# Kernel tuning notes

Measured on AMD Instinct MI355X. Metric: run time of the kernel, lower is better.

## Reference

```python
import jax, jax.numpy as jnp
import numpy as np

EPS = 1e-5  # config.layer_norm_epsilon

def setup_inputs() -> dict:
    key = jax.random.key(0)
    ks = jax.random.split(key, 3)
    B, S, NX, A, H, O = 16, 2048, 1024, 20, 50, 3
    x = jax.random.normal(ks[0], (B, S, NX), dtype=jnp.float32)
    ln_g = jnp.ones((A, NX), jnp.float32)
    ln_b = jnp.zeros((A, NX), jnp.float32)
    W1 = jax.random.normal(ks[1], (A, NX, H), dtype=jnp.float32) * (1.0 / np.sqrt(NX))
    b1 = jnp.zeros((A, H), jnp.float32)
    W2 = jax.random.normal(ks[2], (A, H, O), dtype=jnp.float32) * (1.0 / np.sqrt(H))
    b2 = jnp.zeros((A, O), jnp.float32)
    return {"x": x, "ln_g": ln_g, "ln_b": ln_b, "W1": W1, "b1": b1, "W2": W2, "b2": b2}

def reference(x, ln_g, ln_b, W1, b1, W2, b2):
    B, S, NX = x.shape
    A = ln_g.shape[0]
    # shared normalization (per-token mean/var), per-adapter affine folded into W1
    mu = jnp.mean(x, axis=-1, keepdims=True)
    var = jnp.mean(jnp.square(x - mu), axis=-1, keepdims=True)  # biased, like torch LN
    xn = (x - mu) * jax.lax.rsqrt(var + EPS)                    # [B,S,NX]
    W1g = ln_g[:, :, None] * W1                                 # [A,NX,H], absorbs LN gamma
    off = jnp.einsum('an,anh->ah', ln_b, W1) + b1               # [A,H],   absorbs LN beta
    h = jax.nn.relu(jnp.einsum('bsn,anh->bash', xn, W1g) + off[None, :, None, :])  # [B,A,S,H]
    o = jnp.einsum('bash,aho->baso', h, W2) + b2[None, :, None, :]                 # [B,A,S,3]
    out = o.reshape(B, A, S * o.shape[-1])                      # [B,A,S*3] (row-major == torch view)
    # squash over the adapter/capsule axis (dim=-1 of [B,S*3,A] == axis 1 here)
    sq = jnp.sum(jnp.square(out), axis=1, keepdims=True)
    scale = sq / (1.0 + sq)
    return scale * out * jax.lax.rsqrt(sq)
```

## Files before the change

### kernel.cpp

```cpp
#include <hip/hip_runtime.h>
#include <hip/hip_bf16.h>
#include <stdint.h>


typedef _Float16 h8 __attribute__((ext_vector_type(8)));
typedef float f4 __attribute__((ext_vector_type(4)));
typedef __attribute__((address_space(1))) void gvoid;
typedef __attribute__((address_space(3))) void lvoid;

__device__ __forceinline__ void cp16(const void* g, void* l) {
  __builtin_amdgcn_global_load_lds((gvoid*)g, (lvoid*)l, 16, 0, 0);
}

__global__ __launch_bounds__(256) void pre_kernel(
    const float* __restrict__ x, const float* __restrict__ ln_g,
    const float* __restrict__ ln_b, const float* __restrict__ W1,
    _Float16* __restrict__ wB, float* __restrict__ offpart,
    float* __restrict__ out, _Float16* __restrict__ xn) {
  const int t = threadIdx.x;
  if (blockIdx.x >= 432) {
    const int w = t >> 6, l = t & 63;
    const int tok = (blockIdx.x - 432) * 4 + w;
    const float4* xr = (const float4*)(x + (size_t)tok * 1024);
    float4 v0 = xr[l], v1 = xr[64 + l], v2 = xr[128 + l], v3 = xr[192 + l];
    float s1 = (v0.x + v0.y + v0.z + v0.w) + (v1.x + v1.y + v1.z + v1.w) +
               (v2.x + v2.y + v2.z + v2.w) + (v3.x + v3.y + v3.z + v3.w);
    float s2 = v0.x * v0.x + v0.y * v0.y + v0.z * v0.z + v0.w * v0.w;
    s2 += v1.x * v1.x + v1.y * v1.y + v1.z * v1.z + v1.w * v1.w;
    s2 += v2.x * v2.x + v2.y * v2.y + v2.z * v2.z + v2.w * v2.w;
    s2 += v3.x * v3.x + v3.y * v3.y + v3.z * v3.z + v3.w * v3.w;
#pragma unroll
    for (int m = 32; m > 0; m >>= 1) {
      s1 += __shfl_xor(s1, m);
      s2 += __shfl_xor(s2, m);
    }
    const float mu = s1 * 0.0009765625f;
    const float var = s2 * 0.0009765625f - mu * mu;
    const float inv = rsqrtf(var + 1e-5f);
    uint2* xw = (uint2*)(xn + (size_t)tok * 1024);
    union { _Float16 h[4]; uint2 u; } q;
#define CVT_STORE(V, OFF)                                 \
    q.h[0] = (_Float16)((V.x - mu) * inv);                \
    q.h[1] = (_Float16)((V.y - mu) * inv);                \
    q.h[2] = (_Float16)((V.z - mu) * inv);                \
    q.h[3] = (_Float16)((V.w - mu) * inv);                \
    xw[(OFF) + l] = q.u;
    CVT_STORE(v0, 0)
    CVT_STORE(v1, 64)
    CVT_STORE(v2, 128)
    CVT_STORE(v3, 192)
#undef CVT_STORE
    return;
  }
  if (blockIdx.x >= 320) {
    static const int sa[7] = {2, 5, 7, 10, 12, 15, 17};
    const int idx = blockIdx.x - 320;
    const int ai = idx >> 4, bi = idx & 15;
    float4* dst = (float4*)(out + ((size_t)(bi * 20 + sa[ai])) * 6144);
    const float4 z4 = {0.f, 0.f, 0.f, 0.f};
    for (int i = t; i < 1536; i += 256) dst[i] = z4;
    return;
  }
  const int a = blockIdx.x >> 4, k0 = (blockIdx.x & 15) * 64;
  __shared__ float tw[3200];
  __shared__ float gg[64], bb[64], red[256];
  const float* src = W1 + (size_t)(a * 1024 + k0) * 50;
  for (int i = t; i < 3200; i += 256) tw[i] = src[i];
  if (t < 64) gg[t] = ln_g[a * 1024 + k0 + t];
  else if (t < 128) bb[t - 64] = ln_b[a * 1024 + k0 + (t - 64)];
  __syncthreads();
  const int h = t & 63, q = t >> 6;
  float po = 0.f;
  if (h < 50) {
#pragma unroll
    for (int half = 0; half < 2; ++half) {
      union { _Float16 hh[8]; uint4 u; } pk;
#pragma unroll
      for (int j = 0; j < 8; ++j) {
        const int k = q * 16 + half * 8 + j;
        const float wv = tw[k * 50 + h];
        pk.hh[j] = (_Float16)(gg[k] * wv);
        po += bb[k] * wv;
      }
      *(uint4*)(wB + (size_t)(a * 50 + h) * 1024 + k0 + q * 16 + half * 8) =
          pk.u;
    }
  }
  red[t] = po;
  __syncthreads();
  if (t < 50)
    offpart[(blockIdx.x & 15) * 1024 + a * 50 + t] =
        red[t] + red[64 + t] + red[128 + t] + red[192 + t];
  if (a == 0 && t < 192) {
    const uint4 z = {0, 0, 0, 0};
    *(uint4*)(wB + (size_t)(1000 + (t >> 3)) * 1024 + k0 + (t & 7) * 8) = z;
  }
}

__global__ __launch_bounds__(256, 4) void gemm_kernel(
    const _Float16* __restrict__ xn, const _Float16* __restrict__ wB,
    const float* __restrict__ offpart, const float* __restrict__ b1,
    const float* __restrict__ W2, float* __restrict__ out) {
  __shared__ __align__(16) char smem[36448];
  const int g = blockIdx.x;
  const int xcd = g & 7, i0 = g >> 3;
  const int nb = i0 & 7;
  const int mb = xcd * 32 + (i0 >> 3);
  const int t = threadIdx.x, w = t >> 6, l = t & 63;

  const int a0 = (nb * 128) / 50;
  float* w2s = (float*)(smem + 34048);
  for (int i = t; i < 600; i += 256) {
    const int j = i / 150, a = a0 + j;
    w2s[i] = (a < 20) ? W2[a * 150 + (i - j * 150)] : 0.f;
  }

  const int lr = l >> 3;
  const int ksl = (l & 7) ^ lr;
  const _Float16* gA = xn + (size_t)(mb * 128 + lr) * 1024 + ksl * 8;
  const _Float16* gB = wB + (size_t)(nb * 128 + lr) * 1024 + ksl * 8;

  const int rowA = ((w >> 1) * 64) + (l & 15);
  const int rowB = ((w & 1) * 64) + (l & 15);
  const int kq = l >> 4;
  const int xa = rowA & 7, xb = rowB & 7;
  const char* pA = smem + rowA * 128;
  const char* pB = smem + 16384 + rowB * 128;

  f4 acc[4][4];
  {
    f4 z = {0.f, 0.f, 0.f, 0.f};
#pragma unroll
    for (int mt = 0; mt < 4; ++mt)
#pragma unroll
      for (int nt = 0; nt < 4; ++nt) acc[mt][nt] = z;
  }

  for (int kt = 0; kt < 16; ++kt) {
#pragma unroll
    for (int i = 0; i < 4; ++i) {
      const int chunk = w * 4 + i;
      cp16(gA + (size_t)chunk * 8192 + kt * 64, smem + chunk * 1024);
      cp16(gB + (size_t)chunk * 8192 + kt * 64, smem + 16384 + chunk * 1024);
    }
    __syncthreads();
#pragma unroll
    for (int ks = 0; ks < 2; ++ks) {
      h8 af[4], bf[4];
      const int sl = ks * 4 + kq;
#pragma unroll
      for (int mt = 0; mt < 4; ++mt)
        af[mt] = *(const h8*)(pA + mt * 2048 + ((sl ^ xa) << 4));
#pragma unroll
      for (int nt = 0; nt < 4; ++nt)
        bf[nt] = *(const h8*)(pB + nt * 2048 + ((sl ^ xb) << 4));
#pragma unroll
      for (int mt = 0; mt < 4; ++mt)
#pragma unroll
        for (int nt = 0; nt < 4; ++nt)
          acc[mt][nt] = __builtin_amdgcn_mfma_f32_16x16x32_f16(
              af[mt], bf[nt], acc[mt][nt], 0, 0, 0);
    }
    __syncthreads();
  }

  float offt[4];
  int ncols[4];
#pragma unroll
  for (int nt = 0; nt < 4; ++nt) {
    ncols[nt] = nb * 128 + rowB + nt * 16;
    offt[nt] = (ncols[nt] < 1000) ? b1[ncols[nt]] : 0.f;
  }
#pragma unroll
  for (int c = 0; c < 16; ++c)
#pragma unroll
    for (int nt = 0; nt < 4; ++nt) offt[nt] += offpart[c * 1024 + ncols[nt]];

  const int ml = t >> 2, j = t & 3;
  const int a = a0 + j;
  const int c0 = nb * 128;
  int cs = a * 50, ce = cs + 50;
  if (cs < c0) cs = c0;
  if (ce > c0 + 128) ce = c0 + 128;
  const bool act = (a < 20) && (cs < ce);
  const int lo = cs - c0;
  const int len = act ? (ce - cs) : 0;
  const int h0 = cs - a * 50;
  const float* wrow = w2s + j * 150 + h0 * 3;

  float* hm = (float*)smem;
  const int mrl = (l >> 4) * 4;
  const int ncol = (w & 1) * 64 + (l & 15);
#pragma unroll
  for (int p = 0; p < 2; ++p) {
    if (p) __syncthreads();
    if ((w >> 1) == p) {
#pragma unroll
      for (int mt = 0; mt < 4; ++mt)
#pragma unroll
        for (int nt = 0; nt < 4; ++nt)
#pragma unroll
          for (int r = 0; r < 4; ++r)
            hm[(mrl + mt * 16 + r) * 133 + (ncol + nt * 16)] =
                fmaxf(acc[mt][nt][r] + offt[nt], 0.f);
    }
    __syncthreads();
    if (act) {
      const float* hr = hm + ml * 133 + lo;
      float o0 = 0.f, o1 = 0.f, o2 = 0.f;
      for (int i = 0; i < len; ++i) {
        const float hv = hr[i];
        o0 += hv * wrow[i * 3 + 0];
        o1 += hv * wrow[i * 3 + 1];
        o2 += hv * wrow[i * 3 + 2];
      }
      const int tok = mb * 128 + p * 64 + ml;
      const int b = tok >> 11, s = tok & 2047;
      float* op = out + ((size_t)(b * 20 + a) * 2048 + (size_t)s) * 3;
      if (len == 50) {
        op[0] = o0; op[1] = o1; op[2] = o2;
      } else {
        atomicAdd(op + 0, o0);
        atomicAdd(op + 1, o1);
        atomicAdd(op + 2, o2);
      }
    }
  }
}

__global__ __launch_bounds__(256) void squash_kernel(
    float* __restrict__ out, const float* __restrict__ b2) {
  const int idx = blockIdx.x * 256 + threadIdx.x;
  const int b = idx / 1536;
  const int r4 = idx - b * 1536;
  const int e0 = r4 * 4;
  const int oi0 = e0 % 3;
  const int oi1 = (oi0 + 1) % 3, oi2 = (oi0 + 2) % 3;
  float4 v[20];
  float4 sq = {0.f, 0.f, 0.f, 0.f};
#pragma unroll
  for (int a = 0; a < 20; ++a) {
    float4 t = *(const float4*)(out + ((size_t)(b * 20 + a)) * 6144 + e0);
    t.x += b2[a * 3 + oi0];
    t.y += b2[a * 3 + oi1];
    t.z += b2[a * 3 + oi2];
    t.w += b2[a * 3 + oi0];
    v[a] = t;
    sq.x += t.x * t.x;
    sq.y += t.y * t.y;
    sq.z += t.z * t.z;
    sq.w += t.w * t.w;
  }
  float4 f;
  f.x = sqrtf(sq.x) / (1.f + sq.x);
  f.y = sqrtf(sq.y) / (1.f + sq.y);
  f.z = sqrtf(sq.z) / (1.f + sq.z);
  f.w = sqrtf(sq.w) / (1.f + sq.w);
#pragma unroll
  for (int a = 0; a < 20; ++a) {
    float4 t = v[a];
    t.x *= f.x; t.y *= f.y; t.z *= f.z; t.w *= f.w;
    *(float4*)(out + ((size_t)(b * 20 + a)) * 6144 + e0) = t;
  }
}

extern "C" void kernel_launch(void* const* d_in, const int* in_sizes, int n_in,
                              void* d_out, int out_size, void* d_ws,
                              size_t ws_size, hipStream_t stream) {
  const float* x    = (const float*)d_in[0];
  const float* ln_g = (const float*)d_in[1];
  const float* ln_b = (const float*)d_in[2];
  const float* W1   = (const float*)d_in[3];
  const float* b1   = (const float*)d_in[4];
  const float* W2   = (const float*)d_in[5];
  const float* b2   = (const float*)d_in[6];
  float* out = (float*)d_out;

  char* ws = (char*)d_ws;
  float* offpart = (float*)ws;
  _Float16* wBw  = (_Float16*)(ws + 65536);
  _Float16* xnw  = (_Float16*)(ws + 65536 + 2097152);

  pre_kernel<<<8624, 256, 0, stream>>>(x, ln_g, ln_b, W1, wBw, offpart, out,
                                       xnw);
  gemm_kernel<<<2048, 256, 0, stream>>>(xnw, wBw, offpart, b1, W2, out);
  squash_kernel<<<96, 256, 0, stream>>>(out, b2);
}
```

Before: 302.7 us.

## Fuse squash into GEMM tail via per-row-block completion counters

Adds a per-M-block atomic counter, zeroed by an extra pre_kernel block. The last of the 8 N-blocks to finish a 128-token row block applies b2 and the capsule squash for that block in place. This drops the separate squash kernel launch and its full re-read of the output. The cost is a grid-level atomic, extra syncthreads, and tail work that runs in only one block per row block.

```diff
diff --git a/kernel.cpp b/kernel.cpp
--- a/kernel.cpp
+++ b/kernel.cpp
@@ -16,8 +16,13 @@
     const float* __restrict__ x, const float* __restrict__ ln_g,
     const float* __restrict__ ln_b, const float* __restrict__ W1,
     _Float16* __restrict__ wB, float* __restrict__ offpart,
-    float* __restrict__ out, _Float16* __restrict__ xn) {
+    float* __restrict__ out, _Float16* __restrict__ xn,
+    uint32_t* __restrict__ cnt) {
   const int t = threadIdx.x;
+  if (blockIdx.x >= 8624) {
+    if (cnt) cnt[t] = 0u;
+    return;
+  }
   if (blockIdx.x >= 432) {
     const int w = t >> 6, l = t & 63;
     const int tok = (blockIdx.x - 432) * 4 + w;
@@ -100,7 +105,8 @@
 __global__ __launch_bounds__(256, 4) void gemm_kernel(
     const _Float16* __restrict__ xn, const _Float16* __restrict__ wB,
     const float* __restrict__ offpart, const float* __restrict__ b1,
-    const float* __restrict__ W2, float* __restrict__ out) {
+    const float* __restrict__ W2, float* __restrict__ out,
+    const float* __restrict__ b2, uint32_t* __restrict__ cnt) {
   __shared__ __align__(16) char smem[36448];
   const int g = blockIdx.x;
   const int xcd = g & 7, i0 = g >> 3;
@@ -226,6 +232,32 @@
       }
     }
   }
+
+  if (!cnt) return;
+  __shared__ uint32_t lastflag;
+  __syncthreads();
+  if (t == 0)
+    lastflag = (__hip_atomic_fetch_add(&cnt[mb], 1u, __ATOMIC_ACQ_REL,
+                                       __HIP_MEMORY_SCOPE_AGENT) == 7u);
+  __syncthreads();
+  if (!lastflag) return;
+  const int b = (mb * 128) >> 11;
+  const float* rbase = out + (size_t)b * 122880 + ((mb * 128) & 2047) * 3;
+  for (int col = t; col < 384; col += 256) {
+    const int oi = col % 3;
+    float v[20];
+    float sq = 0.f;
+#pragma unroll
+    for (int a2 = 0; a2 < 20; ++a2) {
+      const float xv = rbase[(size_t)a2 * 6144 + col] + b2[a2 * 3 + oi];
+      v[a2] = xv;
+      sq += xv * xv;
+    }
+    const float f = sqrtf(sq) / (1.f + sq);
+#pragma unroll
+    for (int a2 = 0; a2 < 20; ++a2)
+      ((float*)rbase)[(size_t)a2 * 6144 + col] = v[a2] * f;
+  }
 }
 
 __global__ __launch_bounds__(256) void squash_kernel(
@@ -280,9 +312,14 @@
   float* offpart = (float*)ws;
   _Float16* wBw  = (_Float16*)(ws + 65536);
   _Float16* xnw  = (_Float16*)(ws + 65536 + 2097152);
-
-  pre_kernel<<<8624, 256, 0, stream>>>(x, ln_g, ln_b, W1, wBw, offpart, out,
-                                       xnw);
-  gemm_kernel<<<2048, 256, 0, stream>>>(xnw, wBw, offpart, b1, W2, out);
-  squash_kernel<<<96, 256, 0, stream>>>(out, b2);
-}
+  const size_t CNT_OFF = 65536 + 2097152 + 67108864;
+  uint32_t* cnt = (ws_size >= CNT_OFF + 1024)
+                      ? (uint32_t*)(ws + CNT_OFF)
+                      : (uint32_t*)nullptr;
+
+  pre_kernel<<<cnt ? 8625 : 8624, 256, 0, stream>>>(x, ln_g, ln_b, W1, wBw,
+                                                    offpart, out, xnw, cnt);
+  gemm_kernel<<<2048, 256, 0, stream>>>(xnw, wBw, offpart, b1, W2, out, b2,
+                                        cnt);
+  if (!cnt) squash_kernel<<<96, 256, 0, stream>>>(out, b2);
+}
```

Result: slower. 349.3 us (+15.4%).

## Double-buffer GEMM LDS tiles with smaller K-step to overlap loads and MFMA

Applied to the files above, without the earlier changes.

The GEMM main loop now uses a K-tile of 32 instead of 64 and splits the same LDS region into two buffers. The next tile's global-to-LDS copies are issued before the current tile's MFMAs, and there is one barrier per iteration instead of two. The goal is to hide global load latency behind compute. The cost is twice as many iterations and barriers, a new 64-byte-row XOR swizzle that may raise LDS bank conflicts, and a pipeline that depends on the barrier ordering being correct.

```diff
diff --git a/kernel.cpp b/kernel.cpp
--- a/kernel.cpp
+++ b/kernel.cpp
@@ -115,17 +115,18 @@
     w2s[i] = (a < 20) ? W2[a * 150 + (i - j * 150)] : 0.f;
   }
 
-  const int lr = l >> 3;
-  const int ksl = (l & 7) ^ lr;
-  const _Float16* gA = xn + (size_t)(mb * 128 + lr) * 1024 + ksl * 8;
-  const _Float16* gB = wB + (size_t)(nb * 128 + lr) * 1024 + ksl * 8;
+  const int srow = l >> 2;
+  const int skq = (l & 3) ^ ((l >> 3) & 3);
+  const _Float16* gA = xn + (size_t)(mb * 128 + srow) * 1024 + skq * 8;
+  const _Float16* gB = wB + (size_t)(nb * 128 + srow) * 1024 + skq * 8;
 
   const int rowA = ((w >> 1) * 64) + (l & 15);
   const int rowB = ((w & 1) * 64) + (l & 15);
   const int kq = l >> 4;
-  const int xa = rowA & 7, xb = rowB & 7;
-  const char* pA = smem + rowA * 128;
-  const char* pB = smem + 16384 + rowB * 128;
+  const int xa2 = (rowA >> 1) & 3, xb2 = (rowB >> 1) & 3;
+  const char* pA = smem + rowA * 64;
+  const char* pB = smem + 16384 + rowB * 64;
+  const int qa = (kq ^ xa2) << 4, qb = (kq ^ xb2) << 4;
 
   f4 acc[4][4];
   {
@@ -136,31 +137,40 @@
       for (int nt = 0; nt < 4; ++nt) acc[mt][nt] = z;
   }
 
-  for (int kt = 0; kt < 16; ++kt) {
-#pragma unroll
-    for (int i = 0; i < 4; ++i) {
-      const int chunk = w * 4 + i;
-      cp16(gA + (size_t)chunk * 8192 + kt * 64, smem + chunk * 1024);
-      cp16(gB + (size_t)chunk * 8192 + kt * 64, smem + 16384 + chunk * 1024);
-    }
-    __syncthreads();
-#pragma unroll
-    for (int ks = 0; ks < 2; ++ks) {
-      h8 af[4], bf[4];
-      const int sl = ks * 4 + kq;
-#pragma unroll
-      for (int mt = 0; mt < 4; ++mt)
-        af[mt] = *(const h8*)(pA + mt * 2048 + ((sl ^ xa) << 4));
+#pragma unroll
+  for (int i = 0; i < 2; ++i) {
+    const int c = w * 2 + i;
+    cp16(gA + (size_t)c * 16384, smem + c * 1024);
+    cp16(gB + (size_t)c * 16384, smem + 16384 + c * 1024);
+  }
+  __syncthreads();
+
+#pragma unroll 2
+  for (int kt = 0; kt < 32; ++kt) {
+    const int cur = (kt & 1) << 13;
+    const int nxt = cur ^ 8192;
+    if (kt < 31) {
+#pragma unroll
+      for (int i = 0; i < 2; ++i) {
+        const int c = w * 2 + i;
+        cp16(gA + (size_t)c * 16384 + (kt + 1) * 32, smem + nxt + c * 1024);
+        cp16(gB + (size_t)c * 16384 + (kt + 1) * 32,
+             smem + 16384 + nxt + c * 1024);
+      }
+    }
+    h8 af[4], bf[4];
+#pragma unroll
+    for (int mt = 0; mt < 4; ++mt)
+      af[mt] = *(const h8*)(pA + cur + mt * 1024 + qa);
+#pragma unroll
+    for (int nt = 0; nt < 4; ++nt)
+      bf[nt] = *(const h8*)(pB + cur + nt * 1024 + qb);
+#pragma unroll
+    for (int mt = 0; mt < 4; ++mt)
 #pragma unroll
       for (int nt = 0; nt < 4; ++nt)
-        bf[nt] = *(const h8*)(pB + nt * 2048 + ((sl ^ xb) << 4));
-#pragma unroll
-      for (int mt = 0; mt < 4; ++mt)
-#pragma unroll
-        for (int nt = 0; nt < 4; ++nt)
-          acc[mt][nt] = __builtin_amdgcn_mfma_f32_16x16x32_f16(
-              af[mt], bf[nt], acc[mt][nt], 0, 0, 0);
-    }
+        acc[mt][nt] = __builtin_amdgcn_mfma_f32_16x16x32_f16(
+            af[mt], bf[nt], acc[mt][nt], 0, 0, 0);
     __syncthreads();
   }
 
```

New measurement: 316.2 us. 4.4% more time.
